# Kernel optimization log

Hardware: AMD Instinct MI355X
Metric: run time of the kernel (lower is better)

The kernel has to match this reference:

```python
import jax, jax.numpy as jnp
import numpy as np

HEADS = 16  # matches init_kwargs


def setup_inputs() -> dict:
    key = jax.random.key(0)
    ks = jax.random.split(key, 9)
    N, L, E, D = 2, 2048, 1024, 64
    return {
        "query": jax.random.normal(ks[0], (N, L, E), dtype=jnp.float32),
        "keys": jax.random.normal(ks[1], (N, L, E), dtype=jnp.float32),
        "values": jax.random.normal(ks[2], (N, L, E), dtype=jnp.float32),
        "masks": jax.random.randint(ks[3], (N, 1, 1, L), 0, 2, dtype=jnp.int32),
        "Wq": jax.random.normal(ks[4], (D, D), dtype=jnp.float32) / np.sqrt(D),
        "Wk": jax.random.normal(ks[5], (D, D), dtype=jnp.float32) / np.sqrt(D),
        "Wv": jax.random.normal(ks[6], (D, D), dtype=jnp.float32) / np.sqrt(D),
        "Wo": jax.random.normal(ks[7], (E, E), dtype=jnp.float32) / np.sqrt(E),
        "bo": jax.random.normal(ks[8], (E,), dtype=jnp.float32),
    }


def reference(query, keys, values, masks, Wq, Wk, Wv, Wo, bo):
    N, Lq, E = query.shape
    Lk = keys.shape[1]
    H = HEADS
    D = E // H
    # split heads: [N, L, H, D]
    q = query.reshape(N, Lq, H, D)
    k = keys.reshape(N, Lk, H, D)
    v = values.reshape(N, Lk, H, D)
    # per-head linear projections (weights shared across heads); Linear: x @ W.T
    q = jnp.einsum("nqhd,ed->nqhe", q, Wq)
    k = jnp.einsum("nkhd,ed->nkhe", k, Wk)
    v = jnp.einsum("nkhd,ed->nkhe", v, Wv)
    # scores [N, H, Lq, Lk]
    scores = jnp.einsum("nqhd,nkhd->nhqk", q, k)
    scores = jnp.where(masks == 0, jnp.float32(-1e20), scores)
    # NOTE: original scales by sqrt(embed_size), not sqrt(head_dim)
    attn = jax.nn.softmax(scores / jnp.sqrt(jnp.float32(E)), axis=3)
    out = jnp.einsum("nhqk,nkhd->nqhd", attn, v).reshape(N, Lq, E)
    return out @ Wo.T + bo
```

## Files before the change

kernel.cpp:

```cpp
#include <hip/hip_runtime.h>


typedef __bf16 bf16_t;
typedef __bf16 bf16x4 __attribute__((ext_vector_type(4)));
typedef __bf16 bf16x8 __attribute__((ext_vector_type(8)));
typedef float f32x4 __attribute__((ext_vector_type(4)));
typedef unsigned int u32x4 __attribute__((ext_vector_type(4)));

#define MFMA16(a, b, c) __builtin_amdgcn_mfma_f32_16x16x32_bf16((a), (b), (c), 0, 0, 0)

#define GLOAD_LDS16(gp, lp)                                              \
    __builtin_amdgcn_global_load_lds(                                    \
        (const __attribute__((address_space(1))) void*)(gp),             \
        (__attribute__((address_space(3))) void*)(lp), 16, 0, 0)

__device__ inline bf16x8 cvt8(const float* __restrict__ p) {
    f32x4 a = *(const f32x4*)p;
    f32x4 b = *(const f32x4*)(p + 4);
    bf16x8 r;
    r[0] = (bf16_t)a[0]; r[1] = (bf16_t)a[1];
    r[2] = (bf16_t)a[2]; r[3] = (bf16_t)a[3];
    r[4] = (bf16_t)b[0]; r[5] = (bf16_t)b[1];
    r[6] = (bf16_t)b[2]; r[7] = (bf16_t)b[3];
    return r;
}

__device__ inline bf16x8 cvt8s(const f32x4 a, const f32x4 b) {
    bf16x8 r;
    r[0] = (bf16_t)a[0]; r[1] = (bf16_t)a[1];
    r[2] = (bf16_t)a[2]; r[3] = (bf16_t)a[3];
    r[4] = (bf16_t)b[0]; r[5] = (bf16_t)b[1];
    r[6] = (bf16_t)b[2]; r[7] = (bf16_t)b[3];
    return r;
}

__device__ inline float exp2_fast(float x) {
    float r;
    asm("v_exp_f32 %0, %1" : "=v"(r) : "v"(x));
    return r;
}

__device__ inline unsigned cvt_pk_bf16(float lo, float hi) {
    unsigned r;
    asm("v_cvt_pk_bf16_f32 %0, %1, %2" : "=v"(r) : "v"(lo), "v"(hi));
    return r;
}

__device__ inline void xchg_quads(unsigned &x, unsigned &y) {
    asm("v_permlane32_swap_b32 %0, %1\n\t"
        "v_permlane16_swap_b32 %0, %1"
        : "+v"(x), "+v"(y));
}

__global__ __launch_bounds__(256) void scan_kernel(
    const int* __restrict__ msk, int* __restrict__ excl, int* __restrict__ lmap,
    const float* __restrict__ Wq, const float* __restrict__ Wk,
    const float* __restrict__ Wv,
    bf16_t* __restrict__ Wqb, bf16_t* __restrict__ Wkb, bf16_t* __restrict__ Wvb)
{
    const int t = threadIdx.x;

    if (blockIdx.x >= 2) {
        const int wi = blockIdx.x - 2;
        const float* Ws = (wi == 0) ? Wq : (wi == 1) ? Wk : Wv;
        bf16_t* Wb = (wi == 0) ? Wqb : (wi == 1) ? Wkb : Wvb;
        const float scale = (wi == 0) ? 0.04508422f : 1.0f;
        #pragma unroll
        for (int j = 0; j < 4; j++) {
            int idx = t * 16 + j * 4;
            f32x4 v = *(const f32x4*)&Ws[idx];
            bf16x4 r;
            r[0] = (bf16_t)(v[0] * scale); r[1] = (bf16_t)(v[1] * scale);
            r[2] = (bf16_t)(v[2] * scale); r[3] = (bf16_t)(v[3] * scale);
            *(bf16x4*)&Wb[idx] = r;
        }
        return;
    }

    __shared__ int wsum[4];
    const int n = blockIdx.x;
    const int lane = t & 63, w = t >> 6;
    const int* m = msk + n * 2048;
    int* e = excl + n * 2049;
    int* lm = lmap + n * 2048;

    int v[8], s = 0;
    #pragma unroll
    for (int j = 0; j < 8; j++) { v[j] = (m[t * 8 + j] != 0); s += v[j]; }

    int inc = s;
    #pragma unroll
    for (int d = 1; d < 64; d <<= 1) {
        int o = __shfl_up(inc, d);
        if (lane >= d) inc += o;
    }
    if (lane == 63) wsum[w] = inc;
    __syncthreads();
    int off = 0;
    #pragma unroll
    for (int i = 0; i < 4; i++)
        if (i < w) off += wsum[i];

    int a = off + inc - s;
    #pragma unroll
    for (int j = 0; j < 8; j++) {
        e[t * 8 + j] = a;
        if (v[j]) lm[a] = t * 8 + j;
        a += v[j];
    }
    if (t == 255) e[2048] = a;
}

__global__ __launch_bounds__(256) void qkv_proj_kernel(
    const float* __restrict__ kin, const float* __restrict__ vin,
    const bf16_t* __restrict__ Wkb, const bf16_t* __restrict__ Wvb,
    const float* __restrict__ Wo,
    const int* __restrict__ excl, const int* __restrict__ lmap,
    bf16_t* __restrict__ kc, bf16_t* __restrict__ vcT, bf16_t* __restrict__ Wob)
{
    __shared__ __align__(16) char smem[51200];

    const int t = threadIdx.x;
    const int w = t >> 6, lane = t & 63, quad = lane >> 4, l16 = lane & 15;

    if (blockIdx.y == 2) {
        int idx = blockIdx.x * 1024 + t * 4;
        f32x4 v = *(const f32x4*)&Wo[idx];
        bf16x4 r;
        r[0] = (bf16_t)v[0]; r[1] = (bf16_t)v[1];
        r[2] = (bf16_t)v[2]; r[3] = (bf16_t)v[3];
        *(bf16x4*)&Wob[idx] = r;
        return;
    }

    if (blockIdx.y == 1) {
        bf16_t* Ct = (bf16_t*)smem;
        const int h = blockIdx.x & 15;
        const int ctile = blockIdx.x >> 4;
        const int n = ctile >> 5;
        const int c0 = (ctile & 31) * 64;
        const int Lc = excl[n * 2049 + 2048];
        if (c0 >= Lc) return;

        const int p0 = w * 16 + l16;
        int cs = c0 + p0; if (cs > Lc - 1) cs = Lc - 1;
        const int tg = lmap[n * 2048 + cs];
        const size_t rb = ((size_t)(n * 2048 + tg)) * 1024 + h * 64;

        bf16x8 b0 = cvt8(&vin[rb + quad * 8]);
        bf16x8 b1 = cvt8(&vin[rb + 32 + quad * 8]);

        #pragma unroll
        for (int nt = 0; nt < 4; nt++) {
            bf16x8 a0 = *(const bf16x8*)&Wvb[(nt * 16 + l16) * 64 + quad * 8];
            bf16x8 a1 = *(const bf16x8*)&Wvb[(nt * 16 + l16) * 64 + 32 + quad * 8];
            f32x4 acc = {0.f, 0.f, 0.f, 0.f};
            acc = MFMA16(a0, b0, acc);
            acc = MFMA16(a1, b1, acc);
            #pragma unroll
            for (int r = 0; r < 4; r++)
                Ct[(nt * 16 + quad * 4 + r) * 72 + w * 16 + l16] = (bf16_t)acc[r];
        }
        __syncthreads();
        const int cnt = (Lc - c0 < 64) ? (Lc - c0) : 64;
        const size_t ob2 = ((size_t)(n * 16 + h)) * 131072 + c0;
        #pragma unroll
        for (int pass = 0; pass < 2; pass++) {
            int r = pass * 32 + (t >> 3);
            int cb8 = (t & 7) * 8;
            if (cb8 < cnt) {
                if (cb8 + 8 <= cnt) {
                    *(bf16x8*)&vcT[ob2 + (size_t)r * 2048 + cb8] =
                        *(const bf16x8*)&Ct[r * 72 + cb8];
                } else {
                    for (int q = cb8; q < cnt; q++)
                        vcT[ob2 + (size_t)r * 2048 + q] = Ct[r * 72 + q];
                }
            }
        }
        return;
    }

    if (blockIdx.x >= 512) return;
    const int n = blockIdx.x >> 8;
    const int c0 = (blockIdx.x & 255) * 8;
    const int Lc = excl[n * 2049 + 2048];
    if (c0 >= Lc) return;

    float* Xs = (float*)smem;
    bf16_t* Ct2 = (bf16_t*)(smem + 32768);

    #pragma unroll
    for (int j = 0; j < 8; j++) {
        int br = w * 32 + j * 4;
        int srow = br + (lane >> 4);
        int scol = ((lane & 15) ^ (srow & 15)) * 4;
        int csx = c0 + (srow >> 4); if (csx > Lc - 1) csx = Lc - 1;
        int hs = srow & 15;
        int ls = lmap[n * 2048 + csx];
        GLOAD_LDS16(&kin[((size_t)((n * 2048 + ls) * 16 + hs)) * 64 + scol], &Xs[br * 64]);
    }
    __syncthreads();

    const int rbase = w * 32;
    bf16x8 a[2][2];
    #pragma unroll
    for (int qs = 0; qs < 2; qs++) {
        int row = rbase + qs * 16 + l16;
        const char* rowp = (const char*)Xs + (size_t)row * 256;
        int swb = (row & 15) << 4;
        #pragma unroll
        for (int c = 0; c < 2; c++) {
            f32x4 lo = *(const f32x4*)(rowp + ((c * 128 + quad * 32) ^ swb));
            f32x4 hi = *(const f32x4*)(rowp + ((c * 128 + quad * 32 + 16) ^ swb));
            a[qs][c] = cvt8s(lo, hi);
        }
    }

    f32x4 acc[4][2];
    #pragma unroll
    for (int nt = 0; nt < 4; nt++) {
        bf16x8 b0 = *(const bf16x8*)&Wkb[(nt * 16 + l16) * 64 + quad * 8];
        bf16x8 b1 = *(const bf16x8*)&Wkb[(nt * 16 + l16) * 64 + 32 + quad * 8];
        #pragma unroll
        for (int qs = 0; qs < 2; qs++) {
            f32x4 z = {0.f, 0.f, 0.f, 0.f};
            z = MFMA16(a[qs][0], b0, z);
            z = MFMA16(a[qs][1], b1, z);
            acc[nt][qs] = z;
        }
    }

    #pragma unroll
    for (int nt = 0; nt < 4; nt++)
        #pragma unroll
        for (int qs = 0; qs < 2; qs++)
            #pragma unroll
            for (int r = 0; r < 4; r++)
                Ct2[(rbase + qs * 16 + quad * 4 + r) * 72 + nt * 16 + l16] = (bf16_t)acc[nt][qs][r];
    __syncthreads();

    #pragma unroll
    for (int it = 0; it < 4; it++) {
        int j = it * 32 + (t >> 3);
        bf16x8 val = *(const bf16x8*)&Ct2[j * 72 + (t & 7) * 8];
        int c = c0 + (j >> 4), h2 = j & 15;
        if (c < Lc)
            *(bf16x8*)&kc[(((size_t)(n * 16 + h2)) * 2048 + c) * 64 + (t & 7) * 8] = val;
    }
}

__global__ __launch_bounds__(256) void attn_kernel(
    const float* __restrict__ qin, const bf16_t* __restrict__ Wqb,
    const bf16_t* __restrict__ kc, const bf16_t* __restrict__ vcT,
    const int* __restrict__ excl, bf16_t* __restrict__ ao)
{
    __shared__ __align__(16) char smem[32768];
    bf16_t* KtP = (bf16_t*)smem;
    bf16_t* VtP = (bf16_t*)(smem + 16384);
#define KT(buf, r, c) KtP[(buf) * 4096 + (r) * 64 + (c)]
#define VT(buf, r, c) VtP[(buf) * 4096 + (r) * 64 + (c)]

    const int t = threadIdx.x;
    const int w = t >> 6, lane = t & 63, quad = lane >> 4, l16 = lane & 15;

    const int flat = blockIdx.x;
    const int xcd = flat & 7, slot = flat >> 3;
    const int nh = xcd * 4 + (slot >> 4), qb = slot & 15;
    const int n = nh >> 4, h = nh & 15;
    const size_t nhbase = (size_t)nh * 131072;

    const int Lc = excl[n * 2049 + 2048];
    const int ntiles = (Lc + 63) >> 6;
    const int rbase = w * 32;
    const int qbase = qb * 128 + rbase;

    bf16x8 aq[2][2];
    {
        float* Xq = (float*)smem;
        bf16_t* Qt = (bf16_t*)(smem + 16384);
        const int qrow0 = qb * 128;
        #pragma unroll
        for (int j = 0; j < 8; j++) {
            int br = w * 32 + j * 4;
            int srow = br + (lane >> 4);
            int scol = ((lane & 15) ^ (srow & 15)) * 4;
            GLOAD_LDS16(&qin[((size_t)(n * 2048 + qrow0 + srow)) * 1024 + h * 64 + scol],
                        &Xq[br * 64]);
        }
        __syncthreads();

        bf16x8 a[2][2];
        #pragma unroll
        for (int qs = 0; qs < 2; qs++) {
            int row = rbase + qs * 16 + l16;
            const char* rowp = (const char*)Xq + (size_t)row * 256;
            int swb = (row & 15) << 4;
            #pragma unroll
            for (int c = 0; c < 2; c++) {
                f32x4 lo = *(const f32x4*)(rowp + ((c * 128 + quad * 32) ^ swb));
                f32x4 hi = *(const f32x4*)(rowp + ((c * 128 + quad * 32 + 16) ^ swb));
                a[qs][c] = cvt8s(lo, hi);
            }
        }
        __syncthreads();

        f32x4 pacc[4][2];
        #pragma unroll
        for (int nt = 0; nt < 4; nt++) {
            bf16x8 b0 = *(const bf16x8*)&Wqb[(nt * 16 + l16) * 64 + quad * 8];
            bf16x8 b1 = *(const bf16x8*)&Wqb[(nt * 16 + l16) * 64 + 32 + quad * 8];
            #pragma unroll
            for (int qs = 0; qs < 2; qs++) {
                f32x4 z = {0.f, 0.f, 0.f, 0.f};
                z = MFMA16(a[qs][0], b0, z);
                z = MFMA16(a[qs][1], b1, z);
                pacc[nt][qs] = z;
            }
        }
        #pragma unroll
        for (int nt = 0; nt < 4; nt++)
            #pragma unroll
            for (int qs = 0; qs < 2; qs++)
                #pragma unroll
                for (int r = 0; r < 4; r++) {
                    int row = rbase + qs * 16 + quad * 4 + r;
                    int col = nt * 16 + l16;
                    int byteoff = row * 128 + ((((col >> 3) ^ (row & 7)) << 4) | ((col & 7) << 1));
                    *(bf16_t*)((char*)Qt + byteoff) = (bf16_t)pacc[nt][qs][r];
                }
        __syncthreads();
        #pragma unroll
        for (int qs = 0; qs < 2; qs++) {
            int row = rbase + qs * 16 + l16;
            #pragma unroll
            for (int c = 0; c < 2; c++)
                aq[qs][c] = *(const bf16x8*)((const char*)Qt + row * 128 +
                                             (((c * 4 + quad) ^ (row & 7)) << 4));
        }
        __syncthreads();
    }

    bf16x8 ones;
    #pragma unroll
    for (int j = 0; j < 8; j++) ones[j] = (bf16_t)1.0f;

    f32x4 o[2][4];
    f32x4 acc_l[2];
    #pragma unroll
    for (int qs = 0; qs < 2; qs++) {
        acc_l[qs][0] = 0.f; acc_l[qs][1] = 0.f; acc_l[qs][2] = 0.f; acc_l[qs][3] = 0.f;
        #pragma unroll
        for (int dt = 0; dt < 4; dt++) {
            o[qs][dt][0] = 0.f; o[qs][dt][1] = 0.f; o[qs][dt][2] = 0.f; o[qs][dt][3] = 0.f;
        }
    }

    const int ksrow = lane >> 3;
    const int kscol = ((lane & 7) ^ (lane >> 3)) * 8;
    const int swr = l16 & 7;
    const int ck0 = (quad ^ swr) * 8;
    const int ck1 = ((quad + 4) ^ swr) * 8;

#define STAGE_KV(buf, kn)                                                     \
    {                                                                         \
        _Pragma("unroll")                                                     \
        for (int j = 0; j < 2; j++) {                                         \
            int rb = w * 16 + j * 8;                                          \
            GLOAD_LDS16(&kc[nhbase + (size_t)((kn) + rb + ksrow) * 64 + kscol],\
                        &KT(buf, rb, 0));                                     \
            GLOAD_LDS16(&vcT[nhbase + (size_t)(rb + ksrow) * 2048 + (kn) + kscol],\
                        &VT(buf, rb, 0));                                     \
        }                                                                     \
    }

    STAGE_KV(0, 0);

    for (int i = 0; i < ntiles; i++) {
        const int cb = i & 1, nb = cb ^ 1;
        const int k0 = i * 64;
        __syncthreads();

        if (i + 1 < ntiles) STAGE_KV(nb, k0 + 64);

        f32x4 st[2][4];
        __builtin_amdgcn_s_setprio(1);
        #pragma unroll
        for (int ct = 0; ct < 4; ct++) {
            bf16x8 kb0 = *(const bf16x8*)&KT(cb, ct * 16 + l16, ck0);
            bf16x8 kb1 = *(const bf16x8*)&KT(cb, ct * 16 + l16, ck1);
            #pragma unroll
            for (int qs = 0; qs < 2; qs++) {
                f32x4 acc = {0.f, 0.f, 0.f, 0.f};
                acc = MFMA16(kb0, aq[qs][0], acc);
                acc = MFMA16(kb1, aq[qs][1], acc);
                st[qs][ct] = acc;
            }
        }
        __builtin_amdgcn_s_setprio(0);

        if (k0 + 64 <= Lc) {
            #pragma unroll
            for (int qs = 0; qs < 2; qs++)
                #pragma unroll
                for (int ct = 0; ct < 4; ct++)
                    #pragma unroll
                    for (int r = 0; r < 4; r++)
                        st[qs][ct][r] = exp2_fast(st[qs][ct][r]);
        } else {
            #pragma unroll
            for (int qs = 0; qs < 2; qs++)
                #pragma unroll
                for (int ct = 0; ct < 4; ct++)
                    #pragma unroll
                    for (int r = 0; r < 4; r++) {
                        int kk = k0 + ct * 16 + quad * 4 + r;
                        st[qs][ct][r] = (kk < Lc) ? exp2_fast(st[qs][ct][r]) : 0.0f;
                    }
        }

        bf16x8 bp[2][2];
        #pragma unroll
        for (int qs = 0; qs < 2; qs++) {
            unsigned u[4][2];
            #pragma unroll
            for (int ct = 0; ct < 4; ct++) {
                u[ct][0] = cvt_pk_bf16(st[qs][ct][0], st[qs][ct][1]);
                u[ct][1] = cvt_pk_bf16(st[qs][ct][2], st[qs][ct][3]);
            }
            #pragma unroll
            for (int hh = 0; hh < 2; hh++) {
                unsigned b0 = u[2 * hh][0], b2 = u[2 * hh + 1][0];
                xchg_quads(b0, b2);
                unsigned b1 = u[2 * hh][1], b3 = u[2 * hh + 1][1];
                xchg_quads(b1, b3);
                u32x4 q4 = {b0, b1, b2, b3};
                bp[qs][hh] = __builtin_bit_cast(bf16x8, q4);
            }
        }

        __builtin_amdgcn_s_setprio(1);
        #pragma unroll
        for (int qs = 0; qs < 2; qs++) {
            acc_l[qs] = MFMA16(ones, bp[qs][0], acc_l[qs]);
            acc_l[qs] = MFMA16(ones, bp[qs][1], acc_l[qs]);
        }
        #pragma unroll
        for (int dt = 0; dt < 4; dt++) {
            bf16x8 va0 = *(const bf16x8*)&VT(cb, dt * 16 + l16, ck0);
            bf16x8 va1 = *(const bf16x8*)&VT(cb, dt * 16 + l16, ck1);
            #pragma unroll
            for (int qs = 0; qs < 2; qs++) {
                o[qs][dt] = MFMA16(va0, bp[qs][0], o[qs][dt]);
                o[qs][dt] = MFMA16(va1, bp[qs][1], o[qs][dt]);
            }
        }
        __builtin_amdgcn_s_setprio(0);
    }

    #pragma unroll
    for (int qs = 0; qs < 2; qs++) {
        float inv = 1.0f / acc_l[qs][0];
        const int q = qbase + qs * 16 + l16;
        const size_t base = ((size_t)n * 2048 + q) * 1024 + h * 64;
        #pragma unroll
        for (int dt = 0; dt < 4; dt++) {
            bf16x4 ov;
            #pragma unroll
            for (int r = 0; r < 4; r++) ov[r] = (bf16_t)(o[qs][dt][r] * inv);
            *(bf16x4*)&ao[base + dt * 16 + quad * 4] = ov;
        }
    }
#undef KT
#undef VT
#undef STAGE_KV
}

__global__ __launch_bounds__(256, 3) void out_proj_kernel(
    const bf16_t* __restrict__ X, const bf16_t* __restrict__ Wob,
    const float* __restrict__ bo, float* __restrict__ out)
{
    __shared__ bf16_t Xs[2][128][64];
    __shared__ bf16_t Ws[2][64][64];

    const int t = threadIdx.x;
    const int w = t >> 6, lane = t & 63, quad = lane >> 4, l16 = lane & 15;
    const int Mbase = blockIdx.x * 128;
    const int Nbase = blockIdx.y * 64;
    const int mrow = (w & 1) * 64;
    const int ncol = (w >> 1) * 32;

    const int scol = ((lane & 7) ^ (lane >> 3)) * 8;
    const int swr  = l16 & 7;

    f32x4 acc[4][2];
    #pragma unroll
    for (int mi = 0; mi < 4; mi++)
        #pragma unroll
        for (int ni = 0; ni < 2; ni++) {
            acc[mi][ni][0] = 0.f; acc[mi][ni][1] = 0.f;
            acc[mi][ni][2] = 0.f; acc[mi][ni][3] = 0.f;
        }

    #pragma unroll
    for (int j = 0; j < 4; j++) {
        int br = w * 32 + j * 8;
        GLOAD_LDS16(&X[(size_t)(Mbase + br + (lane >> 3)) * 1024 + scol], &Xs[0][br][0]);
    }
    #pragma unroll
    for (int j = 0; j < 2; j++) {
        int br = w * 16 + j * 8;
        GLOAD_LDS16(&Wob[(size_t)(Nbase + br + (lane >> 3)) * 1024 + scol], &Ws[0][br][0]);
    }

    for (int i = 0; i < 16; i++) {
        const int cb = i & 1, nb = cb ^ 1;
        __syncthreads();

        if (i < 15) {
            const int kn = (i + 1) * 64;
            #pragma unroll
            for (int j = 0; j < 4; j++) {
                int br = w * 32 + j * 8;
                GLOAD_LDS16(&X[(size_t)(Mbase + br + (lane >> 3)) * 1024 + kn + scol],
                            &Xs[nb][br][0]);
            }
            #pragma unroll
            for (int j = 0; j < 2; j++) {
                int br = w * 16 + j * 8;
                GLOAD_LDS16(&Wob[(size_t)(Nbase + br + (lane >> 3)) * 1024 + kn + scol],
                            &Ws[nb][br][0]);
            }
        }

        #pragma unroll
        for (int c = 0; c < 2; c++) {
            bf16x8 bfr[2];
            #pragma unroll
            for (int ni = 0; ni < 2; ni++)
                bfr[ni] = *(const bf16x8*)&Ws[cb][ncol + ni * 16 + l16][((c * 4 + quad) ^ swr) * 8];
            #pragma unroll
            for (int mi = 0; mi < 4; mi++) {
                bf16x8 afr = *(const bf16x8*)&Xs[cb][mrow + mi * 16 + l16][((c * 4 + quad) ^ swr) * 8];
                #pragma unroll
                for (int ni = 0; ni < 2; ni++)
                    acc[mi][ni] = MFMA16(afr, bfr[ni], acc[mi][ni]);
            }
        }
    }

    #pragma unroll
    for (int ni = 0; ni < 2; ni++) {
        float b = bo[Nbase + ncol + ni * 16 + l16];
        #pragma unroll
        for (int mi = 0; mi < 4; mi++) {
            #pragma unroll
            for (int r = 0; r < 4; r++) {
                int row = Mbase + mrow + mi * 16 + quad * 4 + r;
                out[(size_t)row * 1024 + Nbase + ncol + ni * 16 + l16] = acc[mi][ni][r] + b;
            }
        }
    }
}

extern "C" void kernel_launch(void* const* d_in, const int* in_sizes, int n_in,
                              void* d_out, int out_size, void* d_ws, size_t ws_size,
                              hipStream_t stream)
{
    const float* qin = (const float*)d_in[0];
    const float* kin = (const float*)d_in[1];
    const float* vin = (const float*)d_in[2];
    const int*   msk = (const int*)d_in[3];
    const float* Wq  = (const float*)d_in[4];
    const float* Wk  = (const float*)d_in[5];
    const float* Wv  = (const float*)d_in[6];
    const float* Wo  = (const float*)d_in[7];
    const float* bo  = (const float*)d_in[8];
    float* out = (float*)d_out;

    bf16_t* ws  = (bf16_t*)d_ws;
    bf16_t* kc  = ws + 4194304;
    bf16_t* vcT = ws + 8388608;
    bf16_t* ao  = ws + 12582912;
    bf16_t* Wob = ws + 16777216;
    int* excl   = (int*)(ws + 17825792);
    int* lmap   = excl + 4100;
    bf16_t* Wqb = (bf16_t*)(lmap + 4096);
    bf16_t* Wkb = Wqb + 4096;
    bf16_t* Wvb = Wkb + 4096;

    scan_kernel<<<5, 256, 0, stream>>>(msk, excl, lmap, Wq, Wk, Wv, Wqb, Wkb, Wvb);
    qkv_proj_kernel<<<dim3(1024, 3), 256, 0, stream>>>(kin, vin, Wkb, Wvb, Wo,
                                                        excl, lmap, kc, vcT, Wob);
    attn_kernel<<<dim3(512), 256, 0, stream>>>(qin, Wqb, kc, vcT, excl, ao);
    out_proj_kernel<<<dim3(32, 16), 256, 0, stream>>>(ao, Wob, bo, out);
}
```

Before: 155.3 us.

## Load K/V fragments directly from global into registers, dropping LDS staging

Replaces the double-buffered LDS staging of K and V tiles, which used global_load_lds with barriers, with direct per-lane global loads of MFMA fragments into registers. K is double-buffered in registers across a 2-way unrolled loop, and the per-tile __syncthreads calls are removed. This removes LDS traffic and block synchronization, but each of the four waves now loads the same K/V tile independently from global memory and L2. It also raises register pressure and may expose load latency, since V is loaded right before its use.

```diff
diff --git a/kernel.cpp b/kernel.cpp
--- a/kernel.cpp
+++ b/kernel.cpp
@@ -256,10 +256,6 @@
     const int* __restrict__ excl, bf16_t* __restrict__ ao)
 {
     __shared__ __align__(16) char smem[32768];
-    bf16_t* KtP = (bf16_t*)smem;
-    bf16_t* VtP = (bf16_t*)(smem + 16384);
-#define KT(buf, r, c) KtP[(buf) * 4096 + (r) * 64 + (c)]
-#define VT(buf, r, c) VtP[(buf) * 4096 + (r) * 64 + (c)]
 
     const int t = threadIdx.x;
     const int w = t >> 6, lane = t & 63, quad = lane >> 4, l16 = lane & 15;
@@ -338,7 +334,6 @@
                 aq[qs][c] = *(const bf16x8*)((const char*)Qt + row * 128 +
                                              (((c * 4 + quad) ^ (row & 7)) << 4));
         }
-        __syncthreads();
     }
 
     bf16x8 ones;
@@ -356,47 +351,37 @@
         }
     }
 
-    const int ksrow = lane >> 3;
-    const int kscol = ((lane & 7) ^ (lane >> 3)) * 8;
-    const int swr = l16 & 7;
-    const int ck0 = (quad ^ swr) * 8;
-    const int ck1 = ((quad + 4) ^ swr) * 8;
-
-#define STAGE_KV(buf, kn)                                                     \
-    {                                                                         \
-        _Pragma("unroll")                                                     \
-        for (int j = 0; j < 2; j++) {                                         \
-            int rb = w * 16 + j * 8;                                          \
-            GLOAD_LDS16(&kc[nhbase + (size_t)((kn) + rb + ksrow) * 64 + kscol],\
-                        &KT(buf, rb, 0));                                     \
-            GLOAD_LDS16(&vcT[nhbase + (size_t)(rb + ksrow) * 2048 + (kn) + kscol],\
-                        &VT(buf, rb, 0));                                     \
-        }                                                                     \
-    }
-
-    STAGE_KV(0, 0);
-
-    for (int i = 0; i < ntiles; i++) {
-        const int cb = i & 1, nb = cb ^ 1;
-        const int k0 = i * 64;
-        __syncthreads();
-
-        if (i + 1 < ntiles) STAGE_KV(nb, k0 + 64);
-
+    bf16x8 kfA[4][2], kfB[4][2], vf[4][2];
+
+    auto loadK = [&](bf16x8 (&KF)[4][2], int kn) {
+        #pragma unroll
+        for (int ct = 0; ct < 4; ct++)
+            #pragma unroll
+            for (int hh = 0; hh < 2; hh++)
+                KF[ct][hh] = *(const bf16x8*)&kc[nhbase +
+                    (size_t)(kn + ct * 16 + l16) * 64 + hh * 32 + quad * 8];
+    };
+    auto loadV = [&](int kn) {
+        #pragma unroll
+        for (int dt = 0; dt < 4; dt++)
+            #pragma unroll
+            for (int hh = 0; hh < 2; hh++)
+                vf[dt][hh] = *(const bf16x8*)&vcT[nhbase +
+                    (size_t)(dt * 16 + l16) * 2048 + kn + hh * 32 + quad * 8];
+    };
+
+    auto compute = [&](bf16x8 (&KF)[4][2], int k0) {
         f32x4 st[2][4];
         __builtin_amdgcn_s_setprio(1);
         #pragma unroll
-        for (int ct = 0; ct < 4; ct++) {
-            bf16x8 kb0 = *(const bf16x8*)&KT(cb, ct * 16 + l16, ck0);
-            bf16x8 kb1 = *(const bf16x8*)&KT(cb, ct * 16 + l16, ck1);
+        for (int ct = 0; ct < 4; ct++)
             #pragma unroll
             for (int qs = 0; qs < 2; qs++) {
                 f32x4 acc = {0.f, 0.f, 0.f, 0.f};
-                acc = MFMA16(kb0, aq[qs][0], acc);
-                acc = MFMA16(kb1, aq[qs][1], acc);
+                acc = MFMA16(KF[ct][0], aq[qs][0], acc);
+                acc = MFMA16(KF[ct][1], aq[qs][1], acc);
                 st[qs][ct] = acc;
             }
-        }
         __builtin_amdgcn_s_setprio(0);
 
         if (k0 + 64 <= Lc) {
@@ -446,16 +431,26 @@
             acc_l[qs] = MFMA16(ones, bp[qs][1], acc_l[qs]);
         }
         #pragma unroll
-        for (int dt = 0; dt < 4; dt++) {
-            bf16x8 va0 = *(const bf16x8*)&VT(cb, dt * 16 + l16, ck0);
-            bf16x8 va1 = *(const bf16x8*)&VT(cb, dt * 16 + l16, ck1);
+        for (int dt = 0; dt < 4; dt++)
             #pragma unroll
             for (int qs = 0; qs < 2; qs++) {
-                o[qs][dt] = MFMA16(va0, bp[qs][0], o[qs][dt]);
-                o[qs][dt] = MFMA16(va1, bp[qs][1], o[qs][dt]);
-            }
-        }
+                o[qs][dt] = MFMA16(vf[dt][0], bp[qs][0], o[qs][dt]);
+                o[qs][dt] = MFMA16(vf[dt][1], bp[qs][1], o[qs][dt]);
+            }
         __builtin_amdgcn_s_setprio(0);
+    };
+
+    loadK(kfA, 0);
+    for (int i = 0; i < ntiles; i += 2) {
+        const int k0 = i * 64;
+        loadV(k0);
+        if (i + 1 < ntiles) loadK(kfB, k0 + 64);
+        compute(kfA, k0);
+        if (i + 1 < ntiles) {
+            loadV(k0 + 64);
+            if (i + 2 < ntiles) loadK(kfA, k0 + 128);
+            compute(kfB, k0 + 64);
+        }
     }
 
     #pragma unroll
@@ -471,9 +466,6 @@
             *(bf16x4*)&ao[base + dt * 16 + quad * 4] = ov;
         }
     }
-#undef KT
-#undef VT
-#undef STAGE_KV
 }
 
 __global__ __launch_bounds__(256, 3) void out_proj_kernel(
```

New measurement: 195.2 us. 25.6% more time.
